# Performance work log

Hardware: AMD Instinct MI355X
Metric: run time of the kernel (lower is better)

## Reference

```python
import jax, jax.numpy as jnp
import numpy as np

SIZE = 32
NUM_CLASSES = 10
B = 16384
RTOL = 0.01
ATOL = 0.01
MAX_STEPS = 96
H0 = 0.05


def setup_inputs() -> dict:
    key = jax.random.key(0)
    ks = jax.random.split(key, 9)
    p = lambda k, s: 0.1 * jax.random.normal(k, s, dtype=jnp.float32)
    z = lambda n: jnp.zeros((n,), dtype=jnp.float32)
    x = jax.random.normal(ks[0], (B, 2), dtype=jnp.float32)
    # per-sample ODE end times T_i in (0, 3]
    samples = 3.0 * jax.random.uniform(ks[1], (B, 1), dtype=jnp.float32) + 1e-3
    return dict(
        x=x, samples=samples,
        node_w1=p(ks[2], (3, SIZE)), node_b1=z(SIZE),
        node_w2=p(ks[3], (SIZE, SIZE)), node_b2=z(SIZE),
        node_w3=p(ks[4], (SIZE, 2)), node_b3=z(2),
        fc_w=p(ks[5], (2, NUM_CLASSES)), fc_b=z(NUM_CLASSES),
        enc_w1=p(ks[6], (2, SIZE)), enc_b1=z(SIZE),
        enc_w2=p(ks[7], (SIZE, SIZE)), enc_b2=z(SIZE),
        enc_w3=p(ks[8], (SIZE, 2)), enc_b3=z(2),
    )


def _net_forward(x, samples, node_w1, node_b1, node_w2, node_b2, node_w3, node_b3,
                 fc_w, fc_b, enc_w1, enc_b1, enc_w2, enc_b2, enc_w3, enc_b3):
    # Encoder -> (alpha, beta) feed only the external prob_model (no effect on act_vec)
    h = jax.nn.relu(x @ enc_w1 + enc_b1)
    h = jax.nn.relu(h @ enc_w2 + enc_b2)
    ab = h @ enc_w3 + enc_b3
    alpha, beta = jnp.exp(ab[:, 0]), jnp.exp(ab[:, 1])  # unused downstream (side effects only)

    # samples[samples >= 50] = 50
    T = jnp.minimum(samples[:, 0], 50.0)  # [B] per-sample end times

    def f(t, y):  # NODE dynamics; t: [B], y: [B,2]
        zin = jnp.concatenate([t[:, None], y], axis=1)  # [B,3]
        h1 = jax.nn.relu(zin @ node_w1 + node_b1)
        h2 = jax.nn.relu(h1 @ node_w2 + node_b2)
        return h2 @ node_w3 + node_b3  # [B,2]

    def step(carry, _):
        t, y, hstep = carry
        rem = T - t
        active = rem > 1e-8
        hs = jnp.where(active, jnp.minimum(hstep, rem), 0.0)  # never overshoot T
        hb = hs[:, None]
        # Dopri5 (RK45) stages
        k1 = f(t, y)
        k2 = f(t + hs * 0.2, y + hb * (0.2 * k1))
        k3 = f(t + hs * 0.3, y + hb * (3.0 / 40.0 * k1 + 9.0 / 40.0 * k2))
        k4 = f(t + hs * 0.8, y + hb * (44.0 / 45.0 * k1 - 56.0 / 15.0 * k2 + 32.0 / 9.0 * k3))
        k5 = f(t + hs * (8.0 / 9.0), y + hb * (19372.0 / 6561.0 * k1 - 25360.0 / 2187.0 * k2 + 64448.0 / 6561.0 * k3 - 212.0 / 729.0 * k4))
        k6 = f(t + hs, y + hb * (9017.0 / 3168.0 * k1 - 355.0 / 33.0 * k2 + 46732.0 / 5247.0 * k3 + 49.0 / 176.0 * k4 - 5103.0 / 18656.0 * k5))
        y5 = y + hb * (35.0 / 384.0 * k1 + 500.0 / 1113.0 * k3 + 125.0 / 192.0 * k4 - 2187.0 / 6784.0 * k5 + 11.0 / 84.0 * k6)
        k7 = f(t + hs, y5)
        err = hb * (71.0 / 57600.0 * k1 - 71.0 / 16695.0 * k3 + 71.0 / 1920.0 * k4 - 17253.0 / 339200.0 * k5 + 22.0 / 525.0 * k6 - 1.0 / 40.0 * k7)
        scale = ATOL + RTOL * jnp.maximum(jnp.abs(y), jnp.abs(y5))
        en = jnp.sqrt(jnp.mean((err / scale) ** 2, axis=1))  # [B]
        accept = active & (en <= 1.0)
        fac = jnp.clip(0.9 * jnp.maximum(en, 1e-10) ** (-0.2), 0.2, 10.0)
        t_n = jnp.where(accept, t + hs, t)
        y_n = jnp.where(accept[:, None], y5, y)
        h_n = jnp.where(active, hs * fac, hstep)
        return (t_n, y_n, h_n), None

    t0 = jnp.zeros((x.shape[0],), dtype=x.dtype)
    h0 = jnp.full((x.shape[0],), H0, dtype=x.dtype)
    (tF, yF, hF), _ = jax.lax.scan(step, (t0, x, h0), None, length=MAX_STEPS)

    # temp[idx] = flow of x[idx] from t=0 to its own T[idx] (sort/scatter in the
    # original only routes each sample's own interpolated state back to its row)
    act = yF @ fc_w + fc_b  # [B, num_classes]
    return act[None, :, :]  # act_vec: [1, B, num_classes]


def reference(x, samples, node_w1, node_b1, node_w2, node_b2, node_w3, node_b3,
              fc_w, fc_b, enc_w1, enc_b1, enc_w2, enc_b2, enc_w3, enc_b3):
    return _net_forward(x, samples, node_w1, node_b1, node_w2, node_b2, node_w3, node_b3,
                        fc_w, fc_b, enc_w1, enc_b1, enc_w2, enc_b2, enc_w3, enc_b3)
```

## Files before the change

kernel.cpp:

```cpp
#include <hip/hip_runtime.h>
#include <math.h>


#define MAXS 96

typedef float v2f __attribute__((ext_vector_type(2)));

static __device__ __forceinline__ v2f splat(float s){ v2f v; v.x=s; v.y=s; return v; }
static __device__ __forceinline__ v2f vfma(v2f a, v2f b, v2f c){ return __builtin_elementwise_fma(a,b,c); }
static __device__ __forceinline__ v2f vrelu(v2f a){ return __builtin_elementwise_max(a, splat(0.0f)); }

template<int CTRL>
static __device__ __forceinline__ float dppf(float x){
    return __int_as_float(__builtin_amdgcn_update_dpp(0, __float_as_int(x), CTRL, 0xF, 0xF, false));
}
static __device__ __forceinline__ float swz16(float x){
    return __int_as_float(__builtin_amdgcn_ds_swizzle(__float_as_int(x), 0x401F));
}
static __device__ __forceinline__ v2f allreduce32(v2f p){
    p.x += dppf<0xB1>(p.x);  p.y += dppf<0xB1>(p.y);
    p.x += dppf<0x4E>(p.x);  p.y += dppf<0x4E>(p.y);
    p.x += dppf<0x141>(p.x); p.y += dppf<0x141>(p.y);
    p.x += dppf<0x140>(p.x); p.y += dppf<0x140>(p.y);
    p.x += swz16(p.x);       p.y += swz16(p.y);
    return p;
}

__global__ __launch_bounds__(256, 4) void node_kernel(
    const float* __restrict__ x, const float* __restrict__ samples,
    const float* __restrict__ w1, const float* __restrict__ b1,
    const float* __restrict__ w2, const float* __restrict__ b2,
    const float* __restrict__ w3, const float* __restrict__ b3,
    const float* __restrict__ fcw, const float* __restrict__ fcb,
    float* __restrict__ out, int n)
{
    const int tid  = blockIdx.x * blockDim.x + threadIdx.x;
    const int elem = tid >> 5;
    const int m    = tid & 31;
    if (elem >= n) return;

    __shared__ float lds[8 * 36];
    float* slot = &lds[(threadIdx.x >> 5) * 36];

    float w2c[32];
#pragma unroll
    for (int j = 0; j < 32; ++j) w2c[j] = w2[j * 32 + m];
    float w1c0 = w1[ 0 + m], w1c1 = w1[32 + m], w1c2 = w1[64 + m];
    float b1c  = b1[m], b2c = b2[m];
    v2f   w3c; w3c.x = w3[2*m + 0]; w3c.y = w3[2*m + 1];
    v2f   b3c; b3c.x = b3[0]; b3c.y = b3[1];

#pragma unroll
    for (int j = 0; j < 32; ++j) { asm volatile("" : "+v"(w2c[j])); }
    asm volatile("" : "+v"(w1c0), "+v"(w1c1), "+v"(w1c2), "+v"(b1c), "+v"(b2c));
    asm volatile("" : "+v"(w3c));

    v2f y = ((const v2f*)x)[elem];
    float T = fminf(samples[elem], 50.0f);
    float t = 0.0f;
    float h = 0.05f;

    auto f_eval = [&](float tt, v2f z) -> v2f {
        float hv = fmaxf(fmaf(tt, w1c0, fmaf(z.x, w1c1, fmaf(z.y, w1c2, b1c))), 0.0f);

        slot[m] = hv;

        const float4* gp = (const float4*)slot;

        float a0 = b2c, a1 = 0.0f, a2 = 0.0f, a3 = 0.0f;
#pragma unroll
        for (int j = 0; j < 8; j += 4) {
            float4 r0 = gp[j], r1 = gp[j+1], r2 = gp[j+2], r3 = gp[j+3];
            a0 = fmaf(r0.x, w2c[4*j +  0], a0); a1 = fmaf(r0.y, w2c[4*j +  1], a1);
            a2 = fmaf(r0.z, w2c[4*j +  2], a2); a3 = fmaf(r0.w, w2c[4*j +  3], a3);
            a0 = fmaf(r1.x, w2c[4*j +  4], a0); a1 = fmaf(r1.y, w2c[4*j +  5], a1);
            a2 = fmaf(r1.z, w2c[4*j +  6], a2); a3 = fmaf(r1.w, w2c[4*j +  7], a3);
            a0 = fmaf(r2.x, w2c[4*j +  8], a0); a1 = fmaf(r2.y, w2c[4*j +  9], a1);
            a2 = fmaf(r2.z, w2c[4*j + 10], a2); a3 = fmaf(r2.w, w2c[4*j + 11], a3);
            a0 = fmaf(r3.x, w2c[4*j + 12], a0); a1 = fmaf(r3.y, w2c[4*j + 13], a1);
            a2 = fmaf(r3.z, w2c[4*j + 14], a2); a3 = fmaf(r3.w, w2c[4*j + 15], a3);
        }
        float h2 = fmaxf((a0 + a1) + (a2 + a3), 0.0f);

        v2f p = splat(h2) * w3c;
        p = allreduce32(p);
        return p + b3c;
    };

    v2f k1 = f_eval(0.0f, y);

    for (int s = 0; s < MAXS; ++s) {
        float rem = T - t;
        if (!(rem > 1e-8f)) break;
        float hs = fminf(h, rem);
        v2f hb = splat(hs);

        v2f k2 = f_eval(t + hs * 0.2f, vfma(hb, splat(0.2f) * k1, y));
        v2f k3 = f_eval(t + hs * 0.3f,
                 vfma(hb, vfma(splat((float)(3.0/40.0)), k1, splat((float)(9.0/40.0)) * k2), y));
        v2f k4 = f_eval(t + hs * 0.8f,
                 vfma(hb, vfma(splat((float)(44.0/45.0)), k1,
                          vfma(splat((float)(-56.0/15.0)), k2, splat((float)(32.0/9.0)) * k3)), y));
        v2f k5 = f_eval(t + hs * (float)(8.0/9.0),
                 vfma(hb, vfma(splat((float)(19372.0/6561.0)), k1,
                          vfma(splat((float)(-25360.0/2187.0)), k2,
                          vfma(splat((float)(64448.0/6561.0)), k3,
                               splat((float)(-212.0/729.0)) * k4))), y));
        v2f k6 = f_eval(t + hs,
                 vfma(hb, vfma(splat((float)(9017.0/3168.0)), k1,
                          vfma(splat((float)(-355.0/33.0)), k2,
                          vfma(splat((float)(46732.0/5247.0)), k3,
                          vfma(splat((float)(49.0/176.0)), k4,
                               splat((float)(-5103.0/18656.0)) * k5)))), y));
        v2f y5 = vfma(hb, vfma(splat((float)(35.0/384.0)), k1,
                          vfma(splat((float)(500.0/1113.0)), k3,
                          vfma(splat((float)(125.0/192.0)), k4,
                          vfma(splat((float)(-2187.0/6784.0)), k5,
                               splat((float)(11.0/84.0)) * k6)))), y);
        v2f k7 = f_eval(t + hs, y5);

        v2f err = hb * vfma(splat((float)(71.0/57600.0)), k1,
                       vfma(splat((float)(-71.0/16695.0)), k3,
                       vfma(splat((float)(71.0/1920.0)), k4,
                       vfma(splat((float)(-17253.0/339200.0)), k5,
                       vfma(splat((float)(22.0/525.0)), k6,
                            splat((float)(-1.0/40.0)) * k7)))));

        v2f sc = vfma(splat(0.01f),
                 __builtin_elementwise_max(__builtin_elementwise_abs(y),
                                           __builtin_elementwise_abs(y5)), splat(0.01f));
        v2f r = err / sc;
        float en = sqrtf(0.5f * (r.x * r.x + r.y * r.y));

        float fac = fminf(fmaxf(0.9f * exp2f(-0.2f * log2f(fmaxf(en, 1e-10f))), 0.2f), 10.0f);

        bool accept = (en <= 1.0f);
        if (accept) { t += hs; y = y5; }
        k1 = accept ? k7 : k1;
        h = hs * fac;
    }

    if (m < 10) {
        out[10 * elem + m] = fmaf(y.x, fcw[m], fmaf(y.y, fcw[10 + m], fcb[m]));
    }
}

extern "C" void kernel_launch(void* const* d_in, const int* in_sizes, int n_in,
                              void* d_out, int out_size, void* d_ws, size_t ws_size,
                              hipStream_t stream) {
    const float* x   = (const float*)d_in[0];
    const float* sm  = (const float*)d_in[1];
    const float* w1  = (const float*)d_in[2];
    const float* b1  = (const float*)d_in[3];
    const float* w2  = (const float*)d_in[4];
    const float* b2  = (const float*)d_in[5];
    const float* w3  = (const float*)d_in[6];
    const float* b3  = (const float*)d_in[7];
    const float* fcw = (const float*)d_in[8];
    const float* fcb = (const float*)d_in[9];
    float* out = (float*)d_out;

    int n = in_sizes[1];
    const int block = 256;
    long long threads = (long long)n * 32;
    int grid = (int)((threads + block - 1) / block);
    node_kernel<<<grid, block, 0, stream>>>(x, sm, w1, b1, w2, b2, w3, b3,
                                            fcw, fcb, out, n);
}
```

Before: 112.1 us.

## Map each ODE sample to 8 lanes with DPP broadcasts instead of LDS

```diff
diff --git a/kernel.cpp b/kernel.cpp
--- a/kernel.cpp
+++ b/kernel.cpp
@@ -14,19 +14,14 @@
 static __device__ __forceinline__ float dppf(float x){
     return __int_as_float(__builtin_amdgcn_update_dpp(0, __float_as_int(x), CTRL, 0xF, 0xF, false));
 }
-static __device__ __forceinline__ float swz16(float x){
-    return __int_as_float(__builtin_amdgcn_ds_swizzle(__float_as_int(x), 0x401F));
-}
-static __device__ __forceinline__ v2f allreduce32(v2f p){
+static __device__ __forceinline__ v2f dpp_allreduce8(v2f p){
     p.x += dppf<0xB1>(p.x);  p.y += dppf<0xB1>(p.y);
     p.x += dppf<0x4E>(p.x);  p.y += dppf<0x4E>(p.y);
     p.x += dppf<0x141>(p.x); p.y += dppf<0x141>(p.y);
-    p.x += dppf<0x140>(p.x); p.y += dppf<0x140>(p.y);
-    p.x += swz16(p.x);       p.y += swz16(p.y);
     return p;
 }
 
-__global__ __launch_bounds__(256, 4) void node_kernel(
+__global__ __launch_bounds__(256, 2) void node_kernel(
     const float* __restrict__ x, const float* __restrict__ samples,
     const float* __restrict__ w1, const float* __restrict__ b1,
     const float* __restrict__ w2, const float* __restrict__ b2,
@@ -35,25 +30,44 @@
     float* __restrict__ out, int n)
 {
     const int tid  = blockIdx.x * blockDim.x + threadIdx.x;
-    const int elem = tid >> 5;
-    const int m    = tid & 31;
+    const int elem = tid >> 3;
+    const int m    = tid & 7;
     if (elem >= n) return;
+    const int q = m >> 2;
+    const int b = (m < 4) ? m : (7 - m);
+    const int mineC  = 8 * b + 4 * q;
+    const int otherC = 8 * b + 4 * (1 - q);
 
-    __shared__ float lds[8 * 36];
-    float* slot = &lds[(threadIdx.x >> 5) * 36];
-
-    float w2c[32];
+    const v2f* w2v = (const v2f*)w2;
+    v2f w2m[32], w2o[32];
 #pragma unroll
-    for (int j = 0; j < 32; ++j) w2c[j] = w2[j * 32 + m];
-    float w1c0 = w1[ 0 + m], w1c1 = w1[32 + m], w1c2 = w1[64 + m];
-    float b1c  = b1[m], b2c = b2[m];
-    v2f   w3c; w3c.x = w3[2*m + 0]; w3c.y = w3[2*m + 1];
-    v2f   b3c; b3c.x = b3[0]; b3c.y = b3[1];
+    for (int k = 0; k < 16; ++k) {
+#pragma unroll
+        for (int p = 0; p < 2; ++p) {
+            w2m[k*2+p] = w2v[(16*q + k) * 16 + mineC/2  + p];
+            w2o[k*2+p] = w2v[(16*q + k) * 16 + otherC/2 + p];
+        }
+    }
+    float4 w1f0 = ((const float4*)w1)[0*8 + m];
+    float4 w1f1 = ((const float4*)w1)[1*8 + m];
+    float4 w1f2 = ((const float4*)w1)[2*8 + m];
+    float4 b1f  = ((const float4*)b1)[m];
+    v2f w1_0A = {w1f0.x, w1f0.y}, w1_0B = {w1f0.z, w1f0.w};
+    v2f w1_1A = {w1f1.x, w1f1.y}, w1_1B = {w1f1.z, w1f1.w};
+    v2f w1_2A = {w1f2.x, w1f2.y}, w1_2B = {w1f2.z, w1f2.w};
+    v2f b1A   = {b1f.x,  b1f.y }, b1B   = {b1f.z,  b1f.w };
+    const v2f* b2v = (const v2f*)b2;
+    v2f b2m0 = b2v[mineC/2 + 0], b2m1 = b2v[mineC/2 + 1];
+    const v2f* w3v = (const v2f*)w3;
+    v2f w3r0 = w3v[mineC+0], w3r1 = w3v[mineC+1], w3r2 = w3v[mineC+2], w3r3 = w3v[mineC+3];
+    v2f b3c; b3c.x = b3[0]; b3c.y = b3[1];
 
 #pragma unroll
-    for (int j = 0; j < 32; ++j) { asm volatile("" : "+v"(w2c[j])); }
-    asm volatile("" : "+v"(w1c0), "+v"(w1c1), "+v"(w1c2), "+v"(b1c), "+v"(b2c));
-    asm volatile("" : "+v"(w3c));
+    for (int k = 0; k < 32; ++k) { asm volatile("" : "+v"(w2m[k]), "+v"(w2o[k])); }
+    asm volatile("" : "+v"(w1_0A), "+v"(w1_0B), "+v"(w1_1A), "+v"(w1_1B));
+    asm volatile("" : "+v"(w1_2A), "+v"(w1_2B), "+v"(b1A), "+v"(b1B));
+    asm volatile("" : "+v"(b2m0), "+v"(b2m1));
+    asm volatile("" : "+v"(w3r0), "+v"(w3r1), "+v"(w3r2), "+v"(w3r3));
 
     v2f y = ((const v2f*)x)[elem];
     float T = fminf(samples[elem], 50.0f);
@@ -61,29 +75,34 @@
     float h = 0.05f;
 
     auto f_eval = [&](float tt, v2f z) -> v2f {
-        float hv = fmaxf(fmaf(tt, w1c0, fmaf(z.x, w1c1, fmaf(z.y, w1c2, b1c))), 0.0f);
+        v2f hA = vrelu(vfma(splat(tt), w1_0A, vfma(splat(z.x), w1_1A, vfma(splat(z.y), w1_2A, b1A))));
+        v2f hB = vrelu(vfma(splat(tt), w1_0B, vfma(splat(z.x), w1_1B, vfma(splat(z.y), w1_2B, b1B))));
 
-        slot[m] = hv;
+        float g[16];
+        g[ 0]=dppf<0x00>(hA.x); g[ 1]=dppf<0x00>(hA.y); g[ 2]=dppf<0x00>(hB.x); g[ 3]=dppf<0x00>(hB.y);
+        g[ 4]=dppf<0x55>(hA.x); g[ 5]=dppf<0x55>(hA.y); g[ 6]=dppf<0x55>(hB.x); g[ 7]=dppf<0x55>(hB.y);
+        g[ 8]=dppf<0xAA>(hA.x); g[ 9]=dppf<0xAA>(hA.y); g[10]=dppf<0xAA>(hB.x); g[11]=dppf<0xAA>(hB.y);
+        g[12]=dppf<0xFF>(hA.x); g[13]=dppf<0xFF>(hA.y); g[14]=dppf<0xFF>(hB.x); g[15]=dppf<0xFF>(hB.y);
 
-        const float4* gp = (const float4*)slot;
+        v2f am0 = b2m0, am1 = b2m1, ao0 = splat(0.0f), ao1 = splat(0.0f);
+#pragma unroll
+        for (int k = 0; k < 16; ++k) {
+            v2f gk = splat(g[k]);
+            am0 = vfma(gk, w2m[k*2+0], am0);
+            am1 = vfma(gk, w2m[k*2+1], am1);
+            ao0 = vfma(gk, w2o[k*2+0], ao0);
+            ao1 = vfma(gk, w2o[k*2+1], ao1);
+        }
+        v2f x0, x1;
+        x0.x = dppf<0x141>(ao0.x); x0.y = dppf<0x141>(ao0.y);
+        x1.x = dppf<0x141>(ao1.x); x1.y = dppf<0x141>(ao1.y);
+        v2f h2a = vrelu(am0 + x0);
+        v2f h2b = vrelu(am1 + x1);
 
-        float a0 = b2c, a1 = 0.0f, a2 = 0.0f, a3 = 0.0f;
-#pragma unroll
-        for (int j = 0; j < 8; j += 4) {
-            float4 r0 = gp[j], r1 = gp[j+1], r2 = gp[j+2], r3 = gp[j+3];
-            a0 = fmaf(r0.x, w2c[4*j +  0], a0); a1 = fmaf(r0.y, w2c[4*j +  1], a1);
-            a2 = fmaf(r0.z, w2c[4*j +  2], a2); a3 = fmaf(r0.w, w2c[4*j +  3], a3);
-            a0 = fmaf(r1.x, w2c[4*j +  4], a0); a1 = fmaf(r1.y, w2c[4*j +  5], a1);
-            a2 = fmaf(r1.z, w2c[4*j +  6], a2); a3 = fmaf(r1.w, w2c[4*j +  7], a3);
-            a0 = fmaf(r2.x, w2c[4*j +  8], a0); a1 = fmaf(r2.y, w2c[4*j +  9], a1);
-            a2 = fmaf(r2.z, w2c[4*j + 10], a2); a3 = fmaf(r2.w, w2c[4*j + 11], a3);
-            a0 = fmaf(r3.x, w2c[4*j + 12], a0); a1 = fmaf(r3.y, w2c[4*j + 13], a1);
-            a2 = fmaf(r3.z, w2c[4*j + 14], a2); a3 = fmaf(r3.w, w2c[4*j + 15], a3);
-        }
-        float h2 = fmaxf((a0 + a1) + (a2 + a3), 0.0f);
-
-        v2f p = splat(h2) * w3c;
-        p = allreduce32(p);
+        v2f p = vfma(splat(h2a.x), w3r0,
+                vfma(splat(h2a.y), w3r1,
+                vfma(splat(h2b.x), w3r2, splat(h2b.y) * w3r3)));
+        p = dpp_allreduce8(p);
         return p + b3c;
     };
 
@@ -140,8 +159,10 @@
         h = hs * fac;
     }
 
-    if (m < 10) {
-        out[10 * elem + m] = fmaf(y.x, fcw[m], fmaf(y.y, fcw[10 + m], fcb[m]));
+    out[10 * elem + m] = fmaf(y.x, fcw[m], fmaf(y.y, fcw[10 + m], fcb[m]));
+    if (m < 2) {
+        int c = 8 + m;
+        out[10 * elem + c] = fmaf(y.x, fcw[c], fmaf(y.y, fcw[10 + c], fcb[c]));
     }
 }
 
@@ -162,7 +183,7 @@
 
     int n = in_sizes[1];
     const int block = 256;
-    long long threads = (long long)n * 32;
+    long long threads = (long long)n * 8;
     int grid = (int)((threads + block - 1) / block);
     node_kernel<<<grid, block, 0, stream>>>(x, sm, w1, b1, w2, b2, w3, b3,
                                             fcw, fcb, out, n);
```

Result: faster. 102.6 us (-8.5%).

## Map each sample to 16 lanes with DPP-based hidden-layer exchange instead of LDS

Applied to the files above, without the earlier changes.

```diff
diff --git a/kernel.cpp b/kernel.cpp
--- a/kernel.cpp
+++ b/kernel.cpp
@@ -14,19 +14,19 @@
 static __device__ __forceinline__ float dppf(float x){
     return __int_as_float(__builtin_amdgcn_update_dpp(0, __float_as_int(x), CTRL, 0xF, 0xF, false));
 }
-static __device__ __forceinline__ float swz16(float x){
-    return __int_as_float(__builtin_amdgcn_ds_swizzle(__float_as_int(x), 0x401F));
+template<int CTRL>
+static __device__ __forceinline__ v2f dppv(v2f a){
+    v2f r; r.x = dppf<CTRL>(a.x); r.y = dppf<CTRL>(a.y); return r;
 }
-static __device__ __forceinline__ v2f allreduce32(v2f p){
-    p.x += dppf<0xB1>(p.x);  p.y += dppf<0xB1>(p.y);
-    p.x += dppf<0x4E>(p.x);  p.y += dppf<0x4E>(p.y);
-    p.x += dppf<0x141>(p.x); p.y += dppf<0x141>(p.y);
-    p.x += dppf<0x140>(p.x); p.y += dppf<0x140>(p.y);
-    p.x += swz16(p.x);       p.y += swz16(p.y);
+static __device__ __forceinline__ v2f dpp_allreduce16(v2f p){
+    p += dppv<0xB1>(p);
+    p += dppv<0x4E>(p);
+    p += dppv<0x141>(p);
+    p += dppv<0x140>(p);
     return p;
 }
 
-__global__ __launch_bounds__(256, 4) void node_kernel(
+__global__ __launch_bounds__(256, 3) void node_kernel(
     const float* __restrict__ x, const float* __restrict__ samples,
     const float* __restrict__ w1, const float* __restrict__ b1,
     const float* __restrict__ w2, const float* __restrict__ b2,
@@ -35,25 +35,38 @@
     float* __restrict__ out, int n)
 {
     const int tid  = blockIdx.x * blockDim.x + threadIdx.x;
-    const int elem = tid >> 5;
-    const int m    = tid & 31;
+    const int elem = tid >> 4;
+    const int m    = tid & 15;
     if (elem >= n) return;
+    const int p = m >> 3;
+    const int i = m & 7;
+    const int b = (m < 8) ? m : (23 - m);
+    const int ob = (m < 8) ? (8 + m) : (15 - m);
 
-    __shared__ float lds[8 * 36];
-    float* slot = &lds[(threadIdx.x >> 5) * 36];
-
-    float w2c[32];
+    const v2f* w2v = (const v2f*)w2;
+    const int P[8] = {0,1,2,3,7,6,5,4};
+    v2f w2m[16], w2o[16];
 #pragma unroll
-    for (int j = 0; j < 32; ++j) w2c[j] = w2[j * 32 + m];
-    float w1c0 = w1[ 0 + m], w1c1 = w1[32 + m], w1c2 = w1[64 + m];
-    float b1c  = b1[m], b2c = b2[m];
-    v2f   w3c; w3c.x = w3[2*m + 0]; w3c.y = w3[2*m + 1];
-    v2f   b3c; b3c.x = b3[0]; b3c.y = b3[1];
+    for (int j = 0; j < 8; ++j) {
+        int lo = 8*p + (i ^ P[j]);
+        int bb = (p == 0) ? lo : (23 - lo);
+        w2m[2*j+0] = w2v[(2*bb    ) * 16 + b];
+        w2m[2*j+1] = w2v[(2*bb + 1) * 16 + b];
+        w2o[2*j+0] = w2v[(2*bb    ) * 16 + ob];
+        w2o[2*j+1] = w2v[(2*bb + 1) * 16 + ob];
+    }
+    const v2f* w1v = (const v2f*)w1;
+    v2f w1p0 = w1v[0*16 + b], w1p1 = w1v[1*16 + b], w1p2 = w1v[2*16 + b];
+    v2f b1p  = ((const v2f*)b1)[b];
+    v2f b2p  = ((const v2f*)b2)[b];
+    const v2f* w3v = (const v2f*)w3;
+    v2f w3r0 = w3v[2*b], w3r1 = w3v[2*b + 1];
+    v2f b3c; b3c.x = b3[0]; b3c.y = b3[1];
 
 #pragma unroll
-    for (int j = 0; j < 32; ++j) { asm volatile("" : "+v"(w2c[j])); }
-    asm volatile("" : "+v"(w1c0), "+v"(w1c1), "+v"(w1c2), "+v"(b1c), "+v"(b2c));
-    asm volatile("" : "+v"(w3c));
+    for (int k = 0; k < 16; ++k) { asm volatile("" : "+v"(w2m[k]), "+v"(w2o[k])); }
+    asm volatile("" : "+v"(w1p0), "+v"(w1p1), "+v"(w1p2), "+v"(b1p), "+v"(b2p));
+    asm volatile("" : "+v"(w3r0), "+v"(w3r1));
 
     v2f y = ((const v2f*)x)[elem];
     float T = fminf(samples[elem], 50.0f);
@@ -61,30 +74,29 @@
     float h = 0.05f;
 
     auto f_eval = [&](float tt, v2f z) -> v2f {
-        float hv = fmaxf(fmaf(tt, w1c0, fmaf(z.x, w1c1, fmaf(z.y, w1c2, b1c))), 0.0f);
+        v2f hv = vrelu(vfma(splat(tt), w1p0, vfma(splat(z.x), w1p1,
+                       vfma(splat(z.y), w1p2, b1p))));
 
-        slot[m] = hv;
+        v2f g0 = hv;
+        v2f g1 = dppv<0xB1>(g0);
+        v2f g2 = dppv<0x4E>(g0), g3 = dppv<0x4E>(g1);
+        v2f g4 = dppv<0x141>(g0), g5 = dppv<0x141>(g1);
+        v2f g6 = dppv<0x141>(g2), g7 = dppv<0x141>(g3);
 
-        const float4* gp = (const float4*)slot;
+        v2f am = b2p, ao = splat(0.0f);
+#define L2(j, gj) \
+        am = vfma(splat((gj).x), w2m[2*(j)+0], am); \
+        am = vfma(splat((gj).y), w2m[2*(j)+1], am); \
+        ao = vfma(splat((gj).x), w2o[2*(j)+0], ao); \
+        ao = vfma(splat((gj).y), w2o[2*(j)+1], ao);
+        L2(0,g0) L2(1,g1) L2(2,g2) L2(3,g3) L2(4,g4) L2(5,g5) L2(6,g6) L2(7,g7)
+#undef L2
 
-        float a0 = b2c, a1 = 0.0f, a2 = 0.0f, a3 = 0.0f;
-#pragma unroll
-        for (int j = 0; j < 8; j += 4) {
-            float4 r0 = gp[j], r1 = gp[j+1], r2 = gp[j+2], r3 = gp[j+3];
-            a0 = fmaf(r0.x, w2c[4*j +  0], a0); a1 = fmaf(r0.y, w2c[4*j +  1], a1);
-            a2 = fmaf(r0.z, w2c[4*j +  2], a2); a3 = fmaf(r0.w, w2c[4*j +  3], a3);
-            a0 = fmaf(r1.x, w2c[4*j +  4], a0); a1 = fmaf(r1.y, w2c[4*j +  5], a1);
-            a2 = fmaf(r1.z, w2c[4*j +  6], a2); a3 = fmaf(r1.w, w2c[4*j +  7], a3);
-            a0 = fmaf(r2.x, w2c[4*j +  8], a0); a1 = fmaf(r2.y, w2c[4*j +  9], a1);
-            a2 = fmaf(r2.z, w2c[4*j + 10], a2); a3 = fmaf(r2.w, w2c[4*j + 11], a3);
-            a0 = fmaf(r3.x, w2c[4*j + 12], a0); a1 = fmaf(r3.y, w2c[4*j + 13], a1);
-            a2 = fmaf(r3.z, w2c[4*j + 14], a2); a3 = fmaf(r3.w, w2c[4*j + 15], a3);
-        }
-        float h2 = fmaxf((a0 + a1) + (a2 + a3), 0.0f);
+        v2f h2 = vrelu(am + dppv<0x140>(ao));
 
-        v2f p = splat(h2) * w3c;
-        p = allreduce32(p);
-        return p + b3c;
+        v2f q = vfma(splat(h2.x), w3r0, splat(h2.y) * w3r1);
+        q = dpp_allreduce16(q);
+        return q + b3c;
     };
 
     v2f k1 = f_eval(0.0f, y);
@@ -162,7 +174,7 @@
 
     int n = in_sizes[1];
     const int block = 256;
-    long long threads = (long long)n * 32;
+    long long threads = (long long)n * 16;
     int grid = (int)((threads + block - 1) / block);
     node_kernel<<<grid, block, 0, stream>>>(x, sm, w1, b1, w2, b2, w3, b3,
                                             fcw, fcb, out, n);
```

After: 106.9 us. -4.7%, faster.
